# Performance work log

Measured on AMD Instinct MI355X. Metric: run time of the kernel, lower is better.

Reference implementation:

```python
import jax, jax.numpy as jnp
import numpy as np

LEAKY = 0.01   # torch LeakyReLU default negative_slope
BN_EPS = 1e-5  # torch BatchNorm1d default eps


def _batchnorm(x, gamma, beta):
    # train-mode BatchNorm1d: normalize with per-batch biased statistics
    mean = jnp.mean(x, axis=0)
    var = jnp.var(x, axis=0)
    return (x - mean) * jax.lax.rsqrt(var + BN_EPS) * gamma + beta


def setup_inputs() -> dict:
    key = jax.random.key(0)
    ks = jax.random.split(key, 8)
    B, F, depth = 32768, 1, 10
    n_nodes = 2 ** depth  # 1024
    x = jax.random.normal(ks[0], (B, F), jnp.float32)
    prenet_w1 = jax.random.normal(ks[1], (16, F), jnp.float32) * 0.5
    prenet_b1 = jax.random.normal(ks[2], (16,), jnp.float32) * 0.1
    bn1_gamma = jnp.ones((16,), jnp.float32)
    bn1_beta = jnp.zeros((16,), jnp.float32)
    prenet_w2 = jax.random.normal(ks[3], (F, 16), jnp.float32) * 0.25
    prenet_b2 = jax.random.normal(ks[4], (F,), jnp.float32) * 0.1
    bn2_gamma = jnp.ones((F,), jnp.float32)
    bn2_beta = jnp.zeros((F,), jnp.float32)
    fc_w = jax.random.normal(ks[5], (n_nodes, F, F), jnp.float32) * 0.5
    fc_b = jax.random.normal(ks[6], (n_nodes, F), jnp.float32) * 0.1
    return {
        'x': x,
        'prenet_w1': prenet_w1, 'prenet_b1': prenet_b1,
        'bn1_gamma': bn1_gamma, 'bn1_beta': bn1_beta,
        'prenet_w2': prenet_w2, 'prenet_b2': prenet_b2,
        'bn2_gamma': bn2_gamma, 'bn2_beta': bn2_beta,
        'fc_w': fc_w, 'fc_b': fc_b,
    }


def reference(x, prenet_w1, prenet_b1, bn1_gamma, bn1_beta,
              prenet_w2, prenet_b2, bn2_gamma, bn2_beta, fc_w, fc_b):
    # prenet: Linear -> LeakyReLU -> BN -> Linear -> LeakyReLU -> BN
    h = jax.nn.leaky_relu(x @ prenet_w1.T + prenet_b1, LEAKY)
    h = _batchnorm(h, bn1_gamma, bn1_beta)
    h = jax.nn.leaky_relu(h @ prenet_w2.T + prenet_b2, LEAKY)
    x = _batchnorm(h, bn2_gamma, bn2_beta)

    # per-node Linear + sigmoid, fused as one batched GEMM:
    # (B,F) x (n_nodes,F,F) -> (B, n_nodes, F); here F == 1
    d = jax.nn.sigmoid(jnp.einsum('bf,nof->bno', x, fc_w) + fc_b)
    decision = jnp.concatenate([d, 1.0 - d], axis=2)  # (B, n_nodes, 2)

    B = x.shape[0]
    depth = int(np.log2(fc_w.shape[0]))
    mu = jnp.ones((B, 2, 1), x.dtype)
    begin, end = 1, 2
    for n_layer in range(depth):  # small fixed loop over tree depth
        # route parent probs to both children: (B, 2^n, 2)
        nu = jnp.tile(mu[:, begin:, :], (1, 1, 2)) * decision[:, begin:end, :]
        begin, end = end, end + 2 ** (n_layer + 1)
        mu = jnp.concatenate([mu, nu.reshape(B, -1, 1)], axis=1)
    mu = mu[..., 0]           # (B, 2^(depth+1))
    return mu.at[:, 0].set(0.0)
```

## Files before the change

### kernel.cpp

```cpp
#include <hip/hip_runtime.h>

#define LEAKY_S 0.01f
#define BN_EPS 1e-5f
#define LOG2E 1.44269504088896340736f

typedef float f32x2 __attribute__((ext_vector_type(2)));
typedef float f32x4 __attribute__((ext_vector_type(4)));

__device__ __forceinline__ float leaky(float v) { return v >= 0.0f ? v : LEAKY_S * v; }
__device__ __forceinline__ float fast_exp2(float v) { return __builtin_amdgcn_exp2f(v); }
__device__ __forceinline__ float sig2(float z2) {
    return __builtin_amdgcn_rcpf(1.0f + fast_exp2(-z2));
}
__device__ __forceinline__ void st2(float* p, float a, float b) {
    f32x2 v = {a, b}; *(f32x2*)p = v;
}
__device__ __forceinline__ void st_nt2(float* p, float a, float b) {
    f32x2 v = {a, b}; __builtin_nontemporal_store(v, (f32x2*)p);
}
__device__ __forceinline__ void st_nt4(float* p, float a, float b, float c, float d) {
    f32x4 v = {a, b, c, d}; __builtin_nontemporal_store(v, (f32x4*)p);
}

__global__ __launch_bounds__(256) void k_part1(const float* __restrict__ x,
        const float* __restrict__ w1, const float* __restrict__ b1,
        float* __restrict__ p1, int B) {
    float w1r[16], b1r[16], s[16], q[16];
#pragma unroll
    for (int j = 0; j < 16; ++j) { w1r[j] = w1[j]; b1r[j] = b1[j]; s[j] = 0.f; q[j] = 0.f; }
    int tid = threadIdx.x;
    int stride = gridDim.x * 256;
    for (int i = blockIdx.x * 256 + tid; i < B; i += stride) {
        float xv = x[i];
#pragma unroll
        for (int j = 0; j < 16; ++j) {
            float h = leaky(fmaf(xv, w1r[j], b1r[j]));
            s[j] += h; q[j] += h * h;
        }
    }
#pragma unroll
    for (int j = 0; j < 16; ++j) {
        for (int off = 32; off >= 1; off >>= 1) {
            s[j] += __shfl_xor(s[j], off, 64);
            q[j] += __shfl_xor(q[j], off, 64);
        }
    }
    __shared__ float red[4][32];
    int w = tid >> 6, lane = tid & 63;
    if (lane == 0) {
#pragma unroll
        for (int j = 0; j < 16; ++j) { red[w][j] = s[j]; red[w][j + 16] = q[j]; }
    }
    __syncthreads();
    if (tid < 32)
        p1[blockIdx.x * 32 + tid] = red[0][tid] + red[1][tid] + red[2][tid] + red[3][tid];
}

__device__ __forceinline__ void fold_bn1(const float* __restrict__ p1,
        const float* __restrict__ w2, const float* __restrict__ b2,
        const float* __restrict__ g1, const float* __restrict__ be1,
        float* coef, int tid, float invB) {
    float acc = 0.f;
    for (int i = 0; i < 64; ++i) acc += p1[i * 32 + tid];
    float qacc = __shfl(acc, tid + 16, 64);
    float cp = 0.f;
    if (tid < 16) {
        float mean = acc * invB;
        float var  = qacc * invB - mean * mean;
        float inv  = rsqrtf(var + BN_EPS) * g1[tid];
        float sh   = fmaf(-mean, inv, be1[tid]);
        coef[tid] = inv * w2[tid];
        cp = sh * w2[tid];
    }
    for (int off = 8; off >= 1; off >>= 1) cp += __shfl_xor(cp, off, 16);
    if (tid == 0) coef[16] = cp + b2[0];
}

__global__ __launch_bounds__(256) void k_h2f(const float* __restrict__ x,
        const float* __restrict__ w1, const float* __restrict__ b1,
        const float* __restrict__ p1, const float* __restrict__ w2,
        const float* __restrict__ b2, const float* __restrict__ g1,
        const float* __restrict__ be1, float* __restrict__ p2, int B, float invB) {
    __shared__ float coef[17];
    int tid = threadIdx.x;
    if (tid < 32) fold_bn1(p1, w2, b2, g1, be1, coef, tid, invB);
    __syncthreads();
    float w1r[16], b1r[16], ar[16];
#pragma unroll
    for (int j = 0; j < 16; ++j) { w1r[j] = w1[j]; b1r[j] = b1[j]; ar[j] = coef[j]; }
    float c0 = coef[16];
    float s = 0.f, q = 0.f;
    int stride = gridDim.x * 256;
    for (int i = blockIdx.x * 256 + tid; i < B; i += stride) {
        float xv = x[i];
        float acc = c0;
#pragma unroll
        for (int j = 0; j < 16; ++j) {
            float h = leaky(fmaf(xv, w1r[j], b1r[j]));
            acc = fmaf(h, ar[j], acc);
        }
        float h2 = leaky(acc);
        s += h2; q += h2 * h2;
    }
    for (int off = 32; off >= 1; off >>= 1) {
        s += __shfl_xor(s, off, 64);
        q += __shfl_xor(q, off, 64);
    }
    __shared__ float red[4][2];
    int w = tid >> 6, lane = tid & 63;
    if (lane == 0) { red[w][0] = s; red[w][1] = q; }
    __syncthreads();
    if (tid == 0) {
        p2[blockIdx.x * 2 + 0] = red[0][0] + red[1][0] + red[2][0] + red[3][0];
        p2[blockIdx.x * 2 + 1] = red[0][1] + red[1][1] + red[2][1] + red[3][1];
    }
}

__global__ __launch_bounds__(256) void k_tree(const float* __restrict__ x,
        const float* __restrict__ w1, const float* __restrict__ b1,
        const float* __restrict__ w2, const float* __restrict__ b2,
        const float* __restrict__ g1, const float* __restrict__ be1,
        const float* __restrict__ g2, const float* __restrict__ be2,
        const float* __restrict__ fcw, const float* __restrict__ fcb,
        const float* __restrict__ p1, const float* __restrict__ p2,
        float* __restrict__ out, int B, float invB) {
    __shared__ float wl[1024], bl[1024];
    __shared__ float coef[19];
    __shared__ float x2s[8];
    int tid = threadIdx.x;

    for (int i = tid; i < 1024; i += 256) {
        int d;
        if (i < 128)      d = i;
        else if (i < 256) { int o = i - 128; d = 128 + ((o & 1) << 6) + (o >> 1); }
        else if (i < 512) { int o = i - 256; d = 256 + ((((o >> 7) << 1) | (o & 1)) << 6) + ((o & 127) >> 1); }
        else              { int o = i - 512; d = 512 + ((((o >> 7) << 1) | (o & 1)) << 6) + ((o & 127) >> 1); }
        wl[d] = fcw[i] * LOG2E;
        bl[d] = fcb[i] * LOG2E;
    }
    if (tid < 32) {
        fold_bn1(p1, w2, b2, g1, be1, coef, tid, invB);
        if (tid == 31) {
            float s = 0.f, q = 0.f;
            for (int i = 0; i < 64; ++i) { s += p2[2 * i]; q += p2[2 * i + 1]; }
            float mean = s * invB, var = q * invB - mean * mean;
            float inv = rsqrtf(var + BN_EPS) * g2[0];
            coef[17] = inv;
            coef[18] = fmaf(-mean, inv, be2[0]);
        }
    }
    __syncthreads();
    if (tid < 8) {
        int r = blockIdx.x * 8 + tid;
        float xv = (r < B) ? x[r] : 0.f;
        float acc = coef[16];
#pragma unroll
        for (int j = 0; j < 16; ++j) {
            float h = leaky(fmaf(xv, w1[j], b1[j]));
            acc = fmaf(h, coef[j], acc);
        }
        x2s[tid] = fmaf(leaky(acc), coef[17], coef[18]);
    }
    __syncthreads();

    const int w = tid >> 6, lane = tid & 63;
    const int rbase = blockIdx.x * 8 + w * 2;
    float x2[2]; bool act[2]; float* op[2];
#pragma unroll
    for (int rr = 0; rr < 2; ++rr) {
        x2[rr] = x2s[w * 2 + rr];
        act[rr] = (rbase + rr) < B;
        op[rr] = out + (size_t)(rbase + rr) * 2048;
        if (act[rr] && lane == 0) st2(op[rr], 0.f, 1.f);
    }

    float mup[2] = {1.f, 1.f};
#pragma unroll
    for (int l = 1; l <= 6; ++l) {
        const int P = 1 << (l - 1);
        float wv = wl[P + lane], bv = bl[P + lane];
#pragma unroll
        for (int rr = 0; rr < 2; ++rr) {
            float z = fmaf(x2[rr], wv, bv);
            float pz = sig2(z);
            float c0 = mup[rr] * pz, c1 = mup[rr] - c0;
            if (act[rr] && lane < P) {
                if (l >= 5) st_nt2(op[rr] + 2 * (P + lane), c0, c1);
                else        st2(op[rr] + 2 * (P + lane), c0, c1);
            }
            float s0 = __shfl(c0, lane >> 1, 64);
            float s1 = __shfl(c1, lane >> 1, 64);
            mup[rr] = (lane & 1) ? s1 : s0;
        }
    }
    float c2[2][2];
    {
        float wv = wl[64 + lane], bv = bl[64 + lane];
#pragma unroll
        for (int rr = 0; rr < 2; ++rr) {
            float z = fmaf(x2[rr], wv, bv);
            float pz = sig2(z);
            c2[rr][0] = mup[rr] * pz;
            c2[rr][1] = mup[rr] - c2[rr][0];
            if (act[rr]) st_nt2(op[rr] + 128 + 2 * lane, c2[rr][0], c2[rr][1]);
        }
    }
    float c4[2][4];
#pragma unroll
    for (int s = 0; s < 2; ++s) {
        float wv = wl[128 + (s << 6) + lane], bv = bl[128 + (s << 6) + lane];
#pragma unroll
        for (int rr = 0; rr < 2; ++rr) {
            float z = fmaf(x2[rr], wv, bv);
            float pz = sig2(z);
            c4[rr][2 * s]     = c2[rr][s] * pz;
            c4[rr][2 * s + 1] = c2[rr][s] - c4[rr][2 * s];
        }
    }
#pragma unroll
    for (int rr = 0; rr < 2; ++rr)
        if (act[rr])
            st_nt4(op[rr] + 256 + (lane << 2), c4[rr][0], c4[rr][1], c4[rr][2], c4[rr][3]);
    float c8[2][2][4];
#pragma unroll
    for (int j2 = 0; j2 < 2; ++j2) {
        int src = (j2 << 5) + (lane >> 1);
        float wv0 = wl[256 + ((2 * j2) << 6) + lane],     bv0 = bl[256 + ((2 * j2) << 6) + lane];
        float wv1 = wl[256 + ((2 * j2 + 1) << 6) + lane], bv1 = bl[256 + ((2 * j2 + 1) << 6) + lane];
#pragma unroll
        for (int rr = 0; rr < 2; ++rr) {
            float A  = __shfl(c4[rr][0], src, 64);
            float Bv = __shfl(c4[rr][1], src, 64);
            float C  = __shfl(c4[rr][2], src, 64);
            float D  = __shfl(c4[rr][3], src, 64);
            float m0 = (lane & 1) ? C : A;
            float m1 = (lane & 1) ? D : Bv;
            float z0 = fmaf(x2[rr], wv0, bv0);
            float z1 = fmaf(x2[rr], wv1, bv1);
            float p0 = sig2(z0), p1v = sig2(z1);
            c8[rr][j2][0] = m0 * p0;
            c8[rr][j2][1] = m0 - c8[rr][j2][0];
            c8[rr][j2][2] = m1 * p1v;
            c8[rr][j2][3] = m1 - c8[rr][j2][2];
            if (act[rr])
                st_nt4(op[rr] + 512 + (j2 << 8) + (lane << 2),
                       c8[rr][j2][0], c8[rr][j2][1], c8[rr][j2][2], c8[rr][j2][3]);
        }
    }
#pragma unroll
    for (int j = 0; j < 4; ++j) {
        const int j2 = j >> 1;
        int src = ((j & 1) << 5) + (lane >> 1);
        float wv0 = wl[512 + ((2 * j) << 6) + lane],     bv0 = bl[512 + ((2 * j) << 6) + lane];
        float wv1 = wl[512 + ((2 * j + 1) << 6) + lane], bv1 = bl[512 + ((2 * j + 1) << 6) + lane];
#pragma unroll
        for (int rr = 0; rr < 2; ++rr) {
            float A  = __shfl(c8[rr][j2][0], src, 64);
            float Bv = __shfl(c8[rr][j2][1], src, 64);
            float C  = __shfl(c8[rr][j2][2], src, 64);
            float D  = __shfl(c8[rr][j2][3], src, 64);
            float m0 = (lane & 1) ? C : A;
            float m1 = (lane & 1) ? D : Bv;
            float z0 = fmaf(x2[rr], wv0, bv0);
            float z1 = fmaf(x2[rr], wv1, bv1);
            float p0 = sig2(z0), p1v = sig2(z1);
            float a0 = m0 * p0,  a1 = m0 - a0;
            float b0 = m1 * p1v, b1 = m1 - b0;
            if (act[rr])
                st_nt4(op[rr] + 1024 + (j << 8) + (lane << 2), a0, a1, b0, b1);
        }
    }
}

extern "C" void kernel_launch(void* const* d_in, const int* in_sizes, int n_in,
                              void* d_out, int out_size, void* d_ws, size_t ws_size,
                              hipStream_t stream) {
    const float* x   = (const float*)d_in[0];
    const float* w1  = (const float*)d_in[1];
    const float* b1  = (const float*)d_in[2];
    const float* g1  = (const float*)d_in[3];
    const float* be1 = (const float*)d_in[4];
    const float* w2  = (const float*)d_in[5];
    const float* b2  = (const float*)d_in[6];
    const float* g2  = (const float*)d_in[7];
    const float* be2 = (const float*)d_in[8];
    const float* fcw = (const float*)d_in[9];
    const float* fcb = (const float*)d_in[10];
    float* out = (float*)d_out;
    int B = in_sizes[0];
    float invB = 1.0f / (float)B;

    float* ws = (float*)d_ws;
    float* p1 = ws;
    float* p2 = ws + 2048;

    k_part1<<<64, 256, 0, stream>>>(x, w1, b1, p1, B);
    k_h2f  <<<64, 256, 0, stream>>>(x, w1, b1, p1, w2, b2, g1, be1, p2, B, invB);

    int blocks = (B + 7) / 8;
    k_tree<<<blocks, 256, 0, stream>>>(x, w1, b1, w2, b2, g1, be1, g2, be2,
                                       fcw, fcb, p1, p2, out, B, invB);
}
```

Baseline: 63.50 us.

## Amortize k_tree setup over 32 rows per block and fold BN2 into weights

```diff
diff --git a/kernel.cpp b/kernel.cpp
--- a/kernel.cpp
+++ b/kernel.cpp
@@ -29,13 +29,16 @@
 #pragma unroll
     for (int j = 0; j < 16; ++j) { w1r[j] = w1[j]; b1r[j] = b1[j]; s[j] = 0.f; q[j] = 0.f; }
     int tid = threadIdx.x;
-    int stride = gridDim.x * 256;
-    for (int i = blockIdx.x * 256 + tid; i < B; i += stride) {
-        float xv = x[i];
-#pragma unroll
-        for (int j = 0; j < 16; ++j) {
-            float h = leaky(fmaf(xv, w1r[j], b1r[j]));
-            s[j] += h; q[j] += h * h;
+    int i = blockIdx.x * 256 + tid;
+    if (2 * i < B) {
+        f32x2 xv = *(const f32x2*)(x + 2 * i);
+#pragma unroll
+        for (int e = 0; e < 2; ++e) {
+#pragma unroll
+            for (int j = 0; j < 16; ++j) {
+                float h = leaky(fmaf(xv[e], w1r[j], b1r[j]));
+                s[j] += h; q[j] += h * h;
+            }
         }
     }
 #pragma unroll
@@ -80,27 +83,32 @@
         const float* __restrict__ w1, const float* __restrict__ b1,
         const float* __restrict__ p1, const float* __restrict__ w2,
         const float* __restrict__ b2, const float* __restrict__ g1,
-        const float* __restrict__ be1, float* __restrict__ p2, int B, float invB) {
+        const float* __restrict__ be1, float* __restrict__ p2,
+        float* __restrict__ cfws, int B, float invB) {
     __shared__ float coef[17];
     int tid = threadIdx.x;
     if (tid < 32) fold_bn1(p1, w2, b2, g1, be1, coef, tid, invB);
     __syncthreads();
+    if (blockIdx.x == 0 && tid < 17) cfws[tid] = coef[tid];
     float w1r[16], b1r[16], ar[16];
 #pragma unroll
     for (int j = 0; j < 16; ++j) { w1r[j] = w1[j]; b1r[j] = b1[j]; ar[j] = coef[j]; }
     float c0 = coef[16];
     float s = 0.f, q = 0.f;
-    int stride = gridDim.x * 256;
-    for (int i = blockIdx.x * 256 + tid; i < B; i += stride) {
-        float xv = x[i];
-        float acc = c0;
-#pragma unroll
-        for (int j = 0; j < 16; ++j) {
-            float h = leaky(fmaf(xv, w1r[j], b1r[j]));
-            acc = fmaf(h, ar[j], acc);
-        }
-        float h2 = leaky(acc);
-        s += h2; q += h2 * h2;
+    int i = blockIdx.x * 256 + tid;
+    if (2 * i < B) {
+        f32x2 xv = *(const f32x2*)(x + 2 * i);
+#pragma unroll
+        for (int e = 0; e < 2; ++e) {
+            float acc = c0;
+#pragma unroll
+            for (int j = 0; j < 16; ++j) {
+                float h = leaky(fmaf(xv[e], w1r[j], b1r[j]));
+                acc = fmaf(h, ar[j], acc);
+            }
+            float h2 = leaky(acc);
+            s += h2; q += h2 * h2;
+        }
     }
     for (int off = 32; off >= 1; off >>= 1) {
         s += __shfl_xor(s, off, 64);
@@ -118,15 +126,13 @@
 
 __global__ __launch_bounds__(256) void k_tree(const float* __restrict__ x,
         const float* __restrict__ w1, const float* __restrict__ b1,
-        const float* __restrict__ w2, const float* __restrict__ b2,
-        const float* __restrict__ g1, const float* __restrict__ be1,
         const float* __restrict__ g2, const float* __restrict__ be2,
         const float* __restrict__ fcw, const float* __restrict__ fcb,
-        const float* __restrict__ p1, const float* __restrict__ p2,
+        const float* __restrict__ p2, const float* __restrict__ cfws,
         float* __restrict__ out, int B, float invB) {
     __shared__ float wl[1024], bl[1024];
-    __shared__ float coef[19];
-    __shared__ float x2s[8];
+    __shared__ float x2s[32];
+    __shared__ float bn2[2];
     int tid = threadIdx.x;
 
     for (int i = tid; i < 1024; i += 256) {
@@ -135,139 +141,152 @@
         else if (i < 256) { int o = i - 128; d = 128 + ((o & 1) << 6) + (o >> 1); }
         else if (i < 512) { int o = i - 256; d = 256 + ((((o >> 7) << 1) | (o & 1)) << 6) + ((o & 127) >> 1); }
         else              { int o = i - 512; d = 512 + ((((o >> 7) << 1) | (o & 1)) << 6) + ((o & 127) >> 1); }
-        wl[d] = fcw[i] * LOG2E;
-        bl[d] = fcb[i] * LOG2E;
-    }
-    if (tid < 32) {
-        fold_bn1(p1, w2, b2, g1, be1, coef, tid, invB);
-        if (tid == 31) {
-            float s = 0.f, q = 0.f;
-            for (int i = 0; i < 64; ++i) { s += p2[2 * i]; q += p2[2 * i + 1]; }
+        wl[d] = fcw[i];
+        bl[d] = fcb[i];
+    }
+    if (tid < 64) {
+        float s = p2[2 * tid], q = p2[2 * tid + 1];
+        for (int off = 32; off >= 1; off >>= 1) {
+            s += __shfl_xor(s, off, 64);
+            q += __shfl_xor(q, off, 64);
+        }
+        if (tid == 0) {
             float mean = s * invB, var = q * invB - mean * mean;
             float inv = rsqrtf(var + BN_EPS) * g2[0];
-            coef[17] = inv;
-            coef[18] = fmaf(-mean, inv, be2[0]);
-        }
-    }
-    __syncthreads();
-    if (tid < 8) {
-        int r = blockIdx.x * 8 + tid;
+            bn2[0] = inv;
+            bn2[1] = fmaf(-mean, inv, be2[0]);
+        }
+    }
+    __syncthreads();
+    {
+        float s2k = bn2[0] * LOG2E, t2 = bn2[1];
+        for (int i = tid; i < 1024; i += 256) {
+            float wv = wl[i];
+            wl[i] = wv * s2k;
+            bl[i] = fmaf(t2, wv, bl[i]) * LOG2E;
+        }
+    }
+    if (tid < 32) {
+        int r = blockIdx.x * 32 + tid;
         float xv = (r < B) ? x[r] : 0.f;
-        float acc = coef[16];
+        float acc = cfws[16];
 #pragma unroll
         for (int j = 0; j < 16; ++j) {
             float h = leaky(fmaf(xv, w1[j], b1[j]));
-            acc = fmaf(h, coef[j], acc);
-        }
-        x2s[tid] = fmaf(leaky(acc), coef[17], coef[18]);
+            acc = fmaf(h, cfws[j], acc);
+        }
+        x2s[tid] = leaky(acc);
     }
     __syncthreads();
 
     const int w = tid >> 6, lane = tid & 63;
-    const int rbase = blockIdx.x * 8 + w * 2;
-    float x2[2]; bool act[2]; float* op[2];
-#pragma unroll
-    for (int rr = 0; rr < 2; ++rr) {
-        x2[rr] = x2s[w * 2 + rr];
-        act[rr] = (rbase + rr) < B;
-        op[rr] = out + (size_t)(rbase + rr) * 2048;
-        if (act[rr] && lane == 0) st2(op[rr], 0.f, 1.f);
-    }
-
-    float mup[2] = {1.f, 1.f};
-#pragma unroll
-    for (int l = 1; l <= 6; ++l) {
-        const int P = 1 << (l - 1);
-        float wv = wl[P + lane], bv = bl[P + lane];
+    const int rbase = blockIdx.x * 32 + w * 8;
+    for (int rp = 0; rp < 4; ++rp) {
+        const int r0 = rbase + 2 * rp;
+        float x2[2]; bool act[2]; float* op[2];
 #pragma unroll
         for (int rr = 0; rr < 2; ++rr) {
-            float z = fmaf(x2[rr], wv, bv);
-            float pz = sig2(z);
-            float c0 = mup[rr] * pz, c1 = mup[rr] - c0;
-            if (act[rr] && lane < P) {
-                if (l >= 5) st_nt2(op[rr] + 2 * (P + lane), c0, c1);
-                else        st2(op[rr] + 2 * (P + lane), c0, c1);
-            }
-            float s0 = __shfl(c0, lane >> 1, 64);
-            float s1 = __shfl(c1, lane >> 1, 64);
-            mup[rr] = (lane & 1) ? s1 : s0;
-        }
-    }
-    float c2[2][2];
-    {
-        float wv = wl[64 + lane], bv = bl[64 + lane];
-#pragma unroll
-        for (int rr = 0; rr < 2; ++rr) {
-            float z = fmaf(x2[rr], wv, bv);
-            float pz = sig2(z);
-            c2[rr][0] = mup[rr] * pz;
-            c2[rr][1] = mup[rr] - c2[rr][0];
-            if (act[rr]) st_nt2(op[rr] + 128 + 2 * lane, c2[rr][0], c2[rr][1]);
-        }
-    }
-    float c4[2][4];
-#pragma unroll
-    for (int s = 0; s < 2; ++s) {
-        float wv = wl[128 + (s << 6) + lane], bv = bl[128 + (s << 6) + lane];
-#pragma unroll
-        for (int rr = 0; rr < 2; ++rr) {
-            float z = fmaf(x2[rr], wv, bv);
-            float pz = sig2(z);
-            c4[rr][2 * s]     = c2[rr][s] * pz;
-            c4[rr][2 * s + 1] = c2[rr][s] - c4[rr][2 * s];
-        }
-    }
-#pragma unroll
-    for (int rr = 0; rr < 2; ++rr)
-        if (act[rr])
-            st_nt4(op[rr] + 256 + (lane << 2), c4[rr][0], c4[rr][1], c4[rr][2], c4[rr][3]);
-    float c8[2][2][4];
-#pragma unroll
-    for (int j2 = 0; j2 < 2; ++j2) {
-        int src = (j2 << 5) + (lane >> 1);
-        float wv0 = wl[256 + ((2 * j2) << 6) + lane],     bv0 = bl[256 + ((2 * j2) << 6) + lane];
-        float wv1 = wl[256 + ((2 * j2 + 1) << 6) + lane], bv1 = bl[256 + ((2 * j2 + 1) << 6) + lane];
-#pragma unroll
-        for (int rr = 0; rr < 2; ++rr) {
-            float A  = __shfl(c4[rr][0], src, 64);
-            float Bv = __shfl(c4[rr][1], src, 64);
-            float C  = __shfl(c4[rr][2], src, 64);
-            float D  = __shfl(c4[rr][3], src, 64);
-            float m0 = (lane & 1) ? C : A;
-            float m1 = (lane & 1) ? D : Bv;
-            float z0 = fmaf(x2[rr], wv0, bv0);
-            float z1 = fmaf(x2[rr], wv1, bv1);
-            float p0 = sig2(z0), p1v = sig2(z1);
-            c8[rr][j2][0] = m0 * p0;
-            c8[rr][j2][1] = m0 - c8[rr][j2][0];
-            c8[rr][j2][2] = m1 * p1v;
-            c8[rr][j2][3] = m1 - c8[rr][j2][2];
+            x2[rr] = x2s[w * 8 + 2 * rp + rr];
+            act[rr] = (r0 + rr) < B;
+            op[rr] = out + (size_t)(r0 + rr) * 2048;
+            if (act[rr] && lane == 0) st2(op[rr], 0.f, 1.f);
+        }
+
+        float mup[2] = {1.f, 1.f};
+#pragma unroll
+        for (int l = 1; l <= 6; ++l) {
+            const int P = 1 << (l - 1);
+            float wv = wl[P + lane], bv = bl[P + lane];
+#pragma unroll
+            for (int rr = 0; rr < 2; ++rr) {
+                float z = fmaf(x2[rr], wv, bv);
+                float pz = sig2(z);
+                float c0 = mup[rr] * pz, c1 = mup[rr] - c0;
+                if (act[rr] && lane < P) {
+                    if (l >= 5) st_nt2(op[rr] + 2 * (P + lane), c0, c1);
+                    else        st2(op[rr] + 2 * (P + lane), c0, c1);
+                }
+                float s0 = __shfl(c0, lane >> 1, 64);
+                float s1 = __shfl(c1, lane >> 1, 64);
+                mup[rr] = (lane & 1) ? s1 : s0;
+            }
+        }
+        float c2[2][2];
+        {
+            float wv = wl[64 + lane], bv = bl[64 + lane];
+#pragma unroll
+            for (int rr = 0; rr < 2; ++rr) {
+                float z = fmaf(x2[rr], wv, bv);
+                float pz = sig2(z);
+                c2[rr][0] = mup[rr] * pz;
+                c2[rr][1] = mup[rr] - c2[rr][0];
+                if (act[rr]) st_nt2(op[rr] + 128 + 2 * lane, c2[rr][0], c2[rr][1]);
+            }
+        }
+        float c4[2][4];
+#pragma unroll
+        for (int s = 0; s < 2; ++s) {
+            float wv = wl[128 + (s << 6) + lane], bv = bl[128 + (s << 6) + lane];
+#pragma unroll
+            for (int rr = 0; rr < 2; ++rr) {
+                float z = fmaf(x2[rr], wv, bv);
+                float pz = sig2(z);
+                c4[rr][2 * s]     = c2[rr][s] * pz;
+                c4[rr][2 * s + 1] = c2[rr][s] - c4[rr][2 * s];
+            }
+        }
+#pragma unroll
+        for (int rr = 0; rr < 2; ++rr)
             if (act[rr])
-                st_nt4(op[rr] + 512 + (j2 << 8) + (lane << 2),
-                       c8[rr][j2][0], c8[rr][j2][1], c8[rr][j2][2], c8[rr][j2][3]);
-        }
-    }
-#pragma unroll
-    for (int j = 0; j < 4; ++j) {
-        const int j2 = j >> 1;
-        int src = ((j & 1) << 5) + (lane >> 1);
-        float wv0 = wl[512 + ((2 * j) << 6) + lane],     bv0 = bl[512 + ((2 * j) << 6) + lane];
-        float wv1 = wl[512 + ((2 * j + 1) << 6) + lane], bv1 = bl[512 + ((2 * j + 1) << 6) + lane];
-#pragma unroll
-        for (int rr = 0; rr < 2; ++rr) {
-            float A  = __shfl(c8[rr][j2][0], src, 64);
-            float Bv = __shfl(c8[rr][j2][1], src, 64);
-            float C  = __shfl(c8[rr][j2][2], src, 64);
-            float D  = __shfl(c8[rr][j2][3], src, 64);
-            float m0 = (lane & 1) ? C : A;
-            float m1 = (lane & 1) ? D : Bv;
-            float z0 = fmaf(x2[rr], wv0, bv0);
-            float z1 = fmaf(x2[rr], wv1, bv1);
-            float p0 = sig2(z0), p1v = sig2(z1);
-            float a0 = m0 * p0,  a1 = m0 - a0;
-            float b0 = m1 * p1v, b1 = m1 - b0;
-            if (act[rr])
-                st_nt4(op[rr] + 1024 + (j << 8) + (lane << 2), a0, a1, b0, b1);
+                st_nt4(op[rr] + 256 + (lane << 2), c4[rr][0], c4[rr][1], c4[rr][2], c4[rr][3]);
+        float c8[2][2][4];
+#pragma unroll
+        for (int j2 = 0; j2 < 2; ++j2) {
+            int src = (j2 << 5) + (lane >> 1);
+            float wv0 = wl[256 + ((2 * j2) << 6) + lane],     bv0 = bl[256 + ((2 * j2) << 6) + lane];
+            float wv1 = wl[256 + ((2 * j2 + 1) << 6) + lane], bv1 = bl[256 + ((2 * j2 + 1) << 6) + lane];
+#pragma unroll
+            for (int rr = 0; rr < 2; ++rr) {
+                float A  = __shfl(c4[rr][0], src, 64);
+                float Bv = __shfl(c4[rr][1], src, 64);
+                float C  = __shfl(c4[rr][2], src, 64);
+                float D  = __shfl(c4[rr][3], src, 64);
+                float m0 = (lane & 1) ? C : A;
+                float m1 = (lane & 1) ? D : Bv;
+                float z0 = fmaf(x2[rr], wv0, bv0);
+                float z1 = fmaf(x2[rr], wv1, bv1);
+                float p0 = sig2(z0), p1v = sig2(z1);
+                c8[rr][j2][0] = m0 * p0;
+                c8[rr][j2][1] = m0 - c8[rr][j2][0];
+                c8[rr][j2][2] = m1 * p1v;
+                c8[rr][j2][3] = m1 - c8[rr][j2][2];
+                if (act[rr])
+                    st_nt4(op[rr] + 512 + (j2 << 8) + (lane << 2),
+                           c8[rr][j2][0], c8[rr][j2][1], c8[rr][j2][2], c8[rr][j2][3]);
+            }
+        }
+#pragma unroll
+        for (int j = 0; j < 4; ++j) {
+            const int j2 = j >> 1;
+            int src = ((j & 1) << 5) + (lane >> 1);
+            float wv0 = wl[512 + ((2 * j) << 6) + lane],     bv0 = bl[512 + ((2 * j) << 6) + lane];
+            float wv1 = wl[512 + ((2 * j + 1) << 6) + lane], bv1 = bl[512 + ((2 * j + 1) << 6) + lane];
+#pragma unroll
+            for (int rr = 0; rr < 2; ++rr) {
+                float A  = __shfl(c8[rr][j2][0], src, 64);
+                float Bv = __shfl(c8[rr][j2][1], src, 64);
+                float C  = __shfl(c8[rr][j2][2], src, 64);
+                float D  = __shfl(c8[rr][j2][3], src, 64);
+                float m0 = (lane & 1) ? C : A;
+                float m1 = (lane & 1) ? D : Bv;
+                float z0 = fmaf(x2[rr], wv0, bv0);
+                float z1 = fmaf(x2[rr], wv1, bv1);
+                float p0 = sig2(z0), p1v = sig2(z1);
+                float a0 = m0 * p0,  a1 = m0 - a0;
+                float b0 = m1 * p1v, b1 = m1 - b0;
+                if (act[rr])
+                    st_nt4(op[rr] + 1024 + (j << 8) + (lane << 2), a0, a1, b0, b1);
+            }
         }
     }
 }
@@ -293,11 +312,12 @@
     float* ws = (float*)d_ws;
     float* p1 = ws;
     float* p2 = ws + 2048;
+    float* cf = ws + 2176;
 
     k_part1<<<64, 256, 0, stream>>>(x, w1, b1, p1, B);
-    k_h2f  <<<64, 256, 0, stream>>>(x, w1, b1, p1, w2, b2, g1, be1, p2, B, invB);
-
-    int blocks = (B + 7) / 8;
-    k_tree<<<blocks, 256, 0, stream>>>(x, w1, b1, w2, b2, g1, be1, g2, be2,
-                                       fcw, fcb, p1, p2, out, B, invB);
-}
+    k_h2f  <<<64, 256, 0, stream>>>(x, w1, b1, p1, w2, b2, g1, be1, p2, cf, B, invB);
+
+    int blocks = (B + 31) / 32;
+    k_tree<<<blocks, 256, 0, stream>>>(x, w1, b1, g2, be2, fcw, fcb, p2, cf,
+                                       out, B, invB);
+}
```

Result: slower. 66.48 us (+4.7%).
